# Kernel optimization log

Measured on AMD Instinct MI355X. Metric: run time of the kernel, lower is better.

## Reference

```python
import jax, jax.numpy as jnp
import numpy as np

N_NODES = 100000
N_EDGES = 1600000
IN_CH = 128
OUT_CH = 64


def setup_inputs() -> dict:
    key = jax.random.key(0)
    k1, k2, k3 = jax.random.split(key, 3)
    x = jax.random.normal(k1, (N_NODES, IN_CH), dtype=jnp.float32)
    edge_index = jax.random.randint(k2, (2, N_EDGES), 0, N_NODES, dtype=jnp.int32)
    # Glorot-style init for the GCN weight
    W = jax.random.normal(k3, (IN_CH, OUT_CH), dtype=jnp.float32) * (1.0 / np.sqrt(IN_CH))
    b = jnp.zeros((OUT_CH,), dtype=jnp.float32)
    return {"x": x, "edge_index": edge_index, "W": W, "b": b}


def reference(x, edge_index, W, b):
    # GCNConv (PyG semantics): linear transform, add self loops,
    # symmetric deg^{-1/2} normalization, scatter-add aggregation, bias; then ReLU.
    n = x.shape[0]
    h = x @ W  # [N, out]

    loops = jnp.arange(n, dtype=edge_index.dtype)
    row = jnp.concatenate([edge_index[0], loops])  # source nodes
    col = jnp.concatenate([edge_index[1], loops])  # target nodes

    deg = jax.ops.segment_sum(jnp.ones_like(col, dtype=h.dtype), col, num_segments=n)
    deg_inv_sqrt = jnp.where(deg > 0, jax.lax.rsqrt(jnp.maximum(deg, 1e-12)), 0.0)
    norm = deg_inv_sqrt[row] * deg_inv_sqrt[col]  # [E+N]

    msg = h[row] * norm[:, None]  # gather + scale
    out = jax.ops.segment_sum(msg, col, num_segments=n)  # scatter-add
    return jax.nn.relu(out + b)
```

## Files before the change

kernel.cpp:

```cpp
#include <hip/hip_runtime.h>
#include <hip/hip_fp16.h>

#define INC 128
#define OUTC 64
#define MAXBUK 512
#define CAP 6144

typedef __attribute__((ext_vector_type(8))) short short8;
typedef __attribute__((ext_vector_type(4))) float f32x4;

__device__ __forceinline__ ushort f2bf(float f) {
    union { float f; unsigned u; } v; v.f = f;
    unsigned r = v.u + 0x7FFF + ((v.u >> 16) & 1);
    return (ushort)(r >> 16);
}

__global__ __launch_bounds__(512) void buk_fill_kernel(const int* __restrict__ rowi,
                                                       const int* __restrict__ coli,
                                                       int* __restrict__ cursor,
                                                       int* __restrict__ packed,
                                                       int E, int nbuk, int per) {
    __shared__ int lcnt[MAXBUK];
    __shared__ int lbase[MAXBUK];
    int tid = threadIdx.x;
    int c0 = blockIdx.x * per;
    int c1 = min(E, c0 + per);
    for (int t = tid; t < nbuk; t += 512) lcnt[t] = 0;
    __syncthreads();
    for (int e = c0 + tid; e < c1; e += 512)
        atomicAdd(&lcnt[coli[e] >> 8], 1);
    __syncthreads();
    for (int t = tid; t < nbuk; t += 512) {
        int c = lcnt[t];
        if (c) lbase[t] = atomicAdd(&cursor[t], c);
        lcnt[t] = 0;
    }
    __syncthreads();
    for (int e = c0 + tid; e < c1; e += 512) {
        int s = rowi[e], d = coli[e];
        int bk = d >> 8;
        int pos = lbase[bk] + atomicAdd(&lcnt[bk], 1);
        if (pos < CAP)
            packed[(size_t)bk * CAP + pos] = (s << 8) | (d & 255);
    }
}

__global__ __launch_bounds__(1024) void deg_kernel(const int* __restrict__ packed,
                                                   const int* __restrict__ cursor,
                                                   float* __restrict__ dinv, int n) {
    __shared__ int cnt[256];
    int k = blockIdx.x, tid = threadIdx.x;
    if (tid < 256) cnt[tid] = 0;
    __syncthreads();
    int m = min(cursor[k], CAP);
    const int* pk = packed + (size_t)k * CAP;
    for (int e = tid; e < m; e += 1024)
        atomicAdd(&cnt[pk[e] & 255], 1);
    __syncthreads();
    int node = (k << 8) + tid;
    if (tid < 256 && node < n) dinv[node] = rsqrtf(1.0f + (float)cnt[tid]);
}

#define WT_STRIDE 136
__global__ __launch_bounds__(256) void gemm_kernel(
        const float* __restrict__ x, const float* __restrict__ W,
        const float* __restrict__ dinv, __half2* __restrict__ g2, int n) {
    __shared__ ushort WT[OUTC * WT_STRIDE];
    int tid = threadIdx.x;
    #pragma unroll
    for (int i = 0; i < 8; ++i) {
        int idx4 = tid + i * 256;
        float4 v = ((const float4*)W)[idx4];
        int e = idx4 * 4;
        int k = e >> 6, nn = e & 63;
        WT[(nn + 0) * WT_STRIDE + k] = f2bf(v.x);
        WT[(nn + 1) * WT_STRIDE + k] = f2bf(v.y);
        WT[(nn + 2) * WT_STRIDE + k] = f2bf(v.z);
        WT[(nn + 3) * WT_STRIDE + k] = f2bf(v.w);
    }
    __syncthreads();

    int w = tid >> 6, lane = tid & 63;
    int m = lane & 15, quad = lane >> 4;
    int rbase = blockIdx.x * 128 + w * 32;

    short8 afrag[2][4];
    #pragma unroll
    for (int rt = 0; rt < 2; ++rt) {
        int row = rbase + rt * 16 + m;
        #pragma unroll
        for (int kc = 0; kc < 4; ++kc) {
            float4 v0 = make_float4(0.f, 0.f, 0.f, 0.f), v1 = v0;
            if (row < n) {
                const float* p = x + (size_t)row * INC + kc * 32 + quad * 8;
                v0 = *(const float4*)p;
                v1 = *(const float4*)(p + 4);
            }
            short8 a;
            a[0] = (short)f2bf(v0.x); a[1] = (short)f2bf(v0.y);
            a[2] = (short)f2bf(v0.z); a[3] = (short)f2bf(v0.w);
            a[4] = (short)f2bf(v1.x); a[5] = (short)f2bf(v1.y);
            a[6] = (short)f2bf(v1.z); a[7] = (short)f2bf(v1.w);
            afrag[rt][kc] = a;
        }
    }

    f32x4 acc[2][4];
    #pragma unroll
    for (int rt = 0; rt < 2; ++rt)
        #pragma unroll
        for (int nt = 0; nt < 4; ++nt)
            acc[rt][nt] = (f32x4){0.f, 0.f, 0.f, 0.f};

    #pragma unroll
    for (int nt = 0; nt < 4; ++nt) {
        #pragma unroll
        for (int kc = 0; kc < 4; ++kc) {
            short8 bf = *(const short8*)&WT[(nt * 16 + m) * WT_STRIDE + kc * 32 + quad * 8];
            acc[0][nt] = __builtin_amdgcn_mfma_f32_16x16x32_bf16(afrag[0][kc], bf, acc[0][nt], 0, 0, 0);
            acc[1][nt] = __builtin_amdgcn_mfma_f32_16x16x32_bf16(afrag[1][kc], bf, acc[1][nt], 0, 0, 0);
        }
    }

    #pragma unroll
    for (int rt = 0; rt < 2; ++rt) {
        #pragma unroll
        for (int reg = 0; reg < 4; ++reg) {
            int r2 = rbase + rt * 16 + quad * 4 + reg;
            if (r2 < n) {
                float di = dinv[r2];
                #pragma unroll
                for (int nt = 0; nt < 2; ++nt)
                    g2[(size_t)r2 * 32 + nt * 16 + m] =
                        __floats2half2_rn(acc[rt][nt][reg] * di, acc[rt][nt + 2][reg] * di);
            }
        }
    }
}

__global__ __launch_bounds__(1024) void agg_kernel(const int* __restrict__ packed,
                                                   const int* __restrict__ cursor,
                                                   const __half2* __restrict__ g2,
                                                   const float* __restrict__ b,
                                                   float* __restrict__ out, int n) {
    __shared__ int cnt[256];
    __shared__ int sc[256];
    __shared__ int cur[256];
    __shared__ int lcsr[CAP];
    int k = blockIdx.x, tid = threadIdx.x;
    int r0 = k << 8;
    if (tid < 256) cnt[tid] = 0;
    __syncthreads();
    int m = min(cursor[k], CAP);
    const int* pk = packed + (size_t)k * CAP;
    int pe[(CAP + 1023) / 1024];
    int ne = 0;
    for (int e = tid; e < m; e += 1024) {
        int p = pk[e];
        pe[ne++] = p;
        atomicAdd(&cnt[p & 255], 1);
    }
    __syncthreads();
    int c = (tid < 256) ? cnt[tid] : 0;
    if (tid < 256) sc[tid] = c;
    __syncthreads();
    #pragma unroll
    for (int off = 1; off < 256; off <<= 1) {
        int t = (tid >= off && tid < 256) ? sc[tid - off] : 0;
        __syncthreads();
        if (tid < 256) sc[tid] += t;
        __syncthreads();
    }
    if (tid < 256) cur[tid] = sc[tid] - c;
    __syncthreads();
    for (int i = 0; i < ne; ++i) {
        int p = pe[i];
        int pos = atomicAdd(&cur[p & 255], 1);
        lcsr[pos] = (int)(((unsigned)p) >> 8);
    }
    __syncthreads();

    int w = tid >> 6, lane = tid & 63;
    int l = lane & 31, half = lane >> 5;
    const __half2* gl = g2 + l;
    float bx = b[l], by = b[l + 32];
    for (int cl = w; cl < 256; cl += 16) {
        int e1 = sc[cl];
        int nd = cnt[cl];
        int j = e1 - nd;
        float ax = 0.f, ay = 0.f;
        for (; j + 16 <= e1; j += 16) {
            int s0 = lcsr[j + half];
            int s1 = lcsr[j + 2 + half];
            int s2 = lcsr[j + 4 + half];
            int s3 = lcsr[j + 6 + half];
            int s4 = lcsr[j + 8 + half];
            int s5 = lcsr[j + 10 + half];
            int s6 = lcsr[j + 12 + half];
            int s7 = lcsr[j + 14 + half];
            float2 f0 = __half22float2(gl[(size_t)s0 * 32]);
            float2 f1 = __half22float2(gl[(size_t)s1 * 32]);
            float2 f2 = __half22float2(gl[(size_t)s2 * 32]);
            float2 f3 = __half22float2(gl[(size_t)s3 * 32]);
            float2 f4 = __half22float2(gl[(size_t)s4 * 32]);
            float2 f5 = __half22float2(gl[(size_t)s5 * 32]);
            float2 f6 = __half22float2(gl[(size_t)s6 * 32]);
            float2 f7 = __half22float2(gl[(size_t)s7 * 32]);
            ax += ((f0.x + f1.x) + (f2.x + f3.x)) + ((f4.x + f5.x) + (f6.x + f7.x));
            ay += ((f0.y + f1.y) + (f2.y + f3.y)) + ((f4.y + f5.y) + (f6.y + f7.y));
        }
        if (j + 8 <= e1) {
            int s0 = lcsr[j + half];
            int s1 = lcsr[j + 2 + half];
            int s2 = lcsr[j + 4 + half];
            int s3 = lcsr[j + 6 + half];
            float2 f0 = __half22float2(gl[(size_t)s0 * 32]);
            float2 f1 = __half22float2(gl[(size_t)s1 * 32]);
            float2 f2 = __half22float2(gl[(size_t)s2 * 32]);
            float2 f3 = __half22float2(gl[(size_t)s3 * 32]);
            ax += (f0.x + f1.x) + (f2.x + f3.x);
            ay += (f0.y + f1.y) + (f2.y + f3.y);
            j += 8;
        }
        for (; j + 2 <= e1; j += 2) {
            int s = lcsr[j + half];
            float2 f = __half22float2(gl[(size_t)s * 32]);
            ax += f.x; ay += f.y;
        }
        if (j < e1 && half == 0) {
            int s = lcsr[j];
            float2 f = __half22float2(gl[(size_t)s * 32]);
            ax += f.x; ay += f.y;
        }
        ax += __shfl_xor(ax, 32);
        ay += __shfl_xor(ay, 32);
        int node = r0 + cl;
        if (half == 0 && node < n) {
            float2 s = __half22float2(gl[(size_t)node * 32]);
            float di = rsqrtf(1.0f + (float)nd);
            out[(size_t)node * OUTC + l]      = fmaxf((ax + s.x) * di + bx, 0.f);
            out[(size_t)node * OUTC + 32 + l] = fmaxf((ay + s.y) * di + by, 0.f);
        }
    }
}

extern "C" void kernel_launch(void* const* d_in, const int* in_sizes, int n_in,
                              void* d_out, int out_size, void* d_ws, size_t ws_size,
                              hipStream_t stream) {
    const float* x  = (const float*)d_in[0];
    const int*   ei = (const int*)d_in[1];
    const float* W  = (const float*)d_in[2];
    const float* b  = (const float*)d_in[3];
    float* out = (float*)d_out;

    int n = in_sizes[0] / INC;
    int E = in_sizes[1] / 2;
    const int* rowi = ei;
    const int* coli = ei + E;

    int nbuk = (n + 255) >> 8;
    int n_pad = ((n + 255) / 256) * 256;

    char* ws = (char*)d_ws;
    int*     cursor = (int*)ws;                  ws += (size_t)MAXBUK * 4;
    float*   dinv   = (float*)ws;                ws += (size_t)n_pad * 4;
    int*     packed = (int*)ws;                  ws += (size_t)nbuk * CAP * 4;
    __half2* g2     = (__half2*)ws;

    int fblocks = 512;
    int per = (E + fblocks - 1) / fblocks;

    hipMemsetAsync(cursor, 0, (size_t)MAXBUK * 4, stream);
    buk_fill_kernel<<<fblocks, 512, 0, stream>>>(rowi, coli, cursor, packed, E, nbuk, per);
    deg_kernel<<<nbuk, 1024, 0, stream>>>(packed, cursor, dinv, n);
    gemm_kernel<<<(n + 127) / 128, 256, 0, stream>>>(x, W, dinv, g2, n);
    agg_kernel<<<nbuk, 1024, 0, stream>>>(packed, cursor, g2, b, out, n);
}
```

Before: 172.9 us.

## Fuse degree counting into bucket fill and shrink buckets to 128 nodes

Removes the separate degree kernel: global degree counts are now accumulated with global atomics during bucket fill, and the GEMM and aggregation kernels read them directly. Buckets shrink from 256 to 128 nodes, which gives smaller shared-memory CSR tiles, 512-thread aggregation blocks and more blocks for occupancy. The aggregation prefix scan now runs on the precomputed degrees, and gather offsets are pre-scaled to byte offsets in 32-bit arithmetic. This adds 1.6M global atomics into a 100K-entry array, and the lower per-bucket capacity of 3328 edges raises the risk of overflow on skewed inputs.

```diff
diff --git a/kernel.cpp b/kernel.cpp
--- a/kernel.cpp
+++ b/kernel.cpp
@@ -3,8 +3,9 @@
 
 #define INC 128
 #define OUTC 64
-#define MAXBUK 512
-#define CAP 6144
+#define MAXBUK 1024
+#define BNODES 128
+#define CAP 3328
 
 typedef __attribute__((ext_vector_type(8))) short short8;
 typedef __attribute__((ext_vector_type(4))) float f32x4;
@@ -18,6 +19,7 @@
 __global__ __launch_bounds__(512) void buk_fill_kernel(const int* __restrict__ rowi,
                                                        const int* __restrict__ coli,
                                                        int* __restrict__ cursor,
+                                                       int* __restrict__ degG,
                                                        int* __restrict__ packed,
                                                        int E, int nbuk, int per) {
     __shared__ int lcnt[MAXBUK];
@@ -27,8 +29,11 @@
     int c1 = min(E, c0 + per);
     for (int t = tid; t < nbuk; t += 512) lcnt[t] = 0;
     __syncthreads();
-    for (int e = c0 + tid; e < c1; e += 512)
-        atomicAdd(&lcnt[coli[e] >> 8], 1);
+    for (int e = c0 + tid; e < c1; e += 512) {
+        int d = coli[e];
+        atomicAdd(&lcnt[d >> 7], 1);
+        atomicAdd(&degG[d], 1);
+    }
     __syncthreads();
     for (int t = tid; t < nbuk; t += 512) {
         int c = lcnt[t];
@@ -38,33 +43,17 @@
     __syncthreads();
     for (int e = c0 + tid; e < c1; e += 512) {
         int s = rowi[e], d = coli[e];
-        int bk = d >> 8;
+        int bk = d >> 7;
         int pos = lbase[bk] + atomicAdd(&lcnt[bk], 1);
         if (pos < CAP)
-            packed[(size_t)bk * CAP + pos] = (s << 8) | (d & 255);
-    }
-}
-
-__global__ __launch_bounds__(1024) void deg_kernel(const int* __restrict__ packed,
-                                                   const int* __restrict__ cursor,
-                                                   float* __restrict__ dinv, int n) {
-    __shared__ int cnt[256];
-    int k = blockIdx.x, tid = threadIdx.x;
-    if (tid < 256) cnt[tid] = 0;
-    __syncthreads();
-    int m = min(cursor[k], CAP);
-    const int* pk = packed + (size_t)k * CAP;
-    for (int e = tid; e < m; e += 1024)
-        atomicAdd(&cnt[pk[e] & 255], 1);
-    __syncthreads();
-    int node = (k << 8) + tid;
-    if (tid < 256 && node < n) dinv[node] = rsqrtf(1.0f + (float)cnt[tid]);
+            packed[(size_t)bk * CAP + pos] = (s << 8) | (d & 127);
+    }
 }
 
 #define WT_STRIDE 136
 __global__ __launch_bounds__(256) void gemm_kernel(
         const float* __restrict__ x, const float* __restrict__ W,
-        const float* __restrict__ dinv, __half2* __restrict__ g2, int n) {
+        const int* __restrict__ degG, __half2* __restrict__ g2, int n) {
     __shared__ ushort WT[OUTC * WT_STRIDE];
     int tid = threadIdx.x;
     #pragma unroll
@@ -128,7 +117,7 @@
         for (int reg = 0; reg < 4; ++reg) {
             int r2 = rbase + rt * 16 + quad * 4 + reg;
             if (r2 < n) {
-                float di = dinv[r2];
+                float di = rsqrtf(1.0f + (float)degG[r2]);
                 #pragma unroll
                 for (int nt = 0; nt < 2; ++nt)
                     g2[(size_t)r2 * 32 + nt * 16 + m] =
@@ -138,105 +127,103 @@
     }
 }
 
-__global__ __launch_bounds__(1024) void agg_kernel(const int* __restrict__ packed,
-                                                   const int* __restrict__ cursor,
-                                                   const __half2* __restrict__ g2,
-                                                   const float* __restrict__ b,
-                                                   float* __restrict__ out, int n) {
-    __shared__ int cnt[256];
-    __shared__ int sc[256];
-    __shared__ int cur[256];
+__global__ __launch_bounds__(512) void agg_kernel(const int* __restrict__ packed,
+                                                  const int* __restrict__ cursor,
+                                                  const int* __restrict__ degG,
+                                                  const __half2* __restrict__ g2,
+                                                  const float* __restrict__ b,
+                                                  float* __restrict__ out, int n) {
+    __shared__ int cnt[BNODES];
+    __shared__ int sc[BNODES];
+    __shared__ int cur[BNODES];
     __shared__ int lcsr[CAP];
     int k = blockIdx.x, tid = threadIdx.x;
-    int r0 = k << 8;
-    if (tid < 256) cnt[tid] = 0;
-    __syncthreads();
+    int r0 = k << 7;
+    if (tid < BNODES) {
+        int node = r0 + tid;
+        int c = (node < n) ? degG[node] : 0;
+        cnt[tid] = c;
+        sc[tid] = c;
+    }
+    __syncthreads();
+    #pragma unroll
+    for (int off = 1; off < BNODES; off <<= 1) {
+        int t = (tid >= off && tid < BNODES) ? sc[tid - off] : 0;
+        __syncthreads();
+        if (tid < BNODES) sc[tid] += t;
+        __syncthreads();
+    }
+    if (tid < BNODES) cur[tid] = sc[tid] - cnt[tid];
+    __syncthreads();
+
     int m = min(cursor[k], CAP);
     const int* pk = packed + (size_t)k * CAP;
-    int pe[(CAP + 1023) / 1024];
-    int ne = 0;
-    for (int e = tid; e < m; e += 1024) {
+    for (int e = tid; e < m; e += 512) {
         int p = pk[e];
-        pe[ne++] = p;
-        atomicAdd(&cnt[p & 255], 1);
-    }
-    __syncthreads();
-    int c = (tid < 256) ? cnt[tid] : 0;
-    if (tid < 256) sc[tid] = c;
-    __syncthreads();
-    #pragma unroll
-    for (int off = 1; off < 256; off <<= 1) {
-        int t = (tid >= off && tid < 256) ? sc[tid - off] : 0;
-        __syncthreads();
-        if (tid < 256) sc[tid] += t;
-        __syncthreads();
-    }
-    if (tid < 256) cur[tid] = sc[tid] - c;
-    __syncthreads();
-    for (int i = 0; i < ne; ++i) {
-        int p = pe[i];
-        int pos = atomicAdd(&cur[p & 255], 1);
-        lcsr[pos] = (int)(((unsigned)p) >> 8);
+        int pos = atomicAdd(&cur[p & 127], 1);
+        if (pos < CAP)
+            lcsr[pos] = (int)((((unsigned)p) >> 8) << 7);
     }
     __syncthreads();
 
     int w = tid >> 6, lane = tid & 63;
     int l = lane & 31, half = lane >> 5;
-    const __half2* gl = g2 + l;
+    const char* gbase = (const char*)g2;
+    unsigned lo4 = (unsigned)l * 4u;
     float bx = b[l], by = b[l + 32];
-    for (int cl = w; cl < 256; cl += 16) {
+    for (int cl = w; cl < BNODES; cl += 8) {
         int e1 = sc[cl];
         int nd = cnt[cl];
         int j = e1 - nd;
         float ax = 0.f, ay = 0.f;
         for (; j + 16 <= e1; j += 16) {
-            int s0 = lcsr[j + half];
-            int s1 = lcsr[j + 2 + half];
-            int s2 = lcsr[j + 4 + half];
-            int s3 = lcsr[j + 6 + half];
-            int s4 = lcsr[j + 8 + half];
-            int s5 = lcsr[j + 10 + half];
-            int s6 = lcsr[j + 12 + half];
-            int s7 = lcsr[j + 14 + half];
-            float2 f0 = __half22float2(gl[(size_t)s0 * 32]);
-            float2 f1 = __half22float2(gl[(size_t)s1 * 32]);
-            float2 f2 = __half22float2(gl[(size_t)s2 * 32]);
-            float2 f3 = __half22float2(gl[(size_t)s3 * 32]);
-            float2 f4 = __half22float2(gl[(size_t)s4 * 32]);
-            float2 f5 = __half22float2(gl[(size_t)s5 * 32]);
-            float2 f6 = __half22float2(gl[(size_t)s6 * 32]);
-            float2 f7 = __half22float2(gl[(size_t)s7 * 32]);
+            unsigned o0 = (unsigned)lcsr[j + half]      + lo4;
+            unsigned o1 = (unsigned)lcsr[j + 2 + half]  + lo4;
+            unsigned o2 = (unsigned)lcsr[j + 4 + half]  + lo4;
+            unsigned o3 = (unsigned)lcsr[j + 6 + half]  + lo4;
+            unsigned o4 = (unsigned)lcsr[j + 8 + half]  + lo4;
+            unsigned o5 = (unsigned)lcsr[j + 10 + half] + lo4;
+            unsigned o6 = (unsigned)lcsr[j + 12 + half] + lo4;
+            unsigned o7 = (unsigned)lcsr[j + 14 + half] + lo4;
+            float2 f0 = __half22float2(*(const __half2*)(gbase + o0));
+            float2 f1 = __half22float2(*(const __half2*)(gbase + o1));
+            float2 f2 = __half22float2(*(const __half2*)(gbase + o2));
+            float2 f3 = __half22float2(*(const __half2*)(gbase + o3));
+            float2 f4 = __half22float2(*(const __half2*)(gbase + o4));
+            float2 f5 = __half22float2(*(const __half2*)(gbase + o5));
+            float2 f6 = __half22float2(*(const __half2*)(gbase + o6));
+            float2 f7 = __half22float2(*(const __half2*)(gbase + o7));
             ax += ((f0.x + f1.x) + (f2.x + f3.x)) + ((f4.x + f5.x) + (f6.x + f7.x));
             ay += ((f0.y + f1.y) + (f2.y + f3.y)) + ((f4.y + f5.y) + (f6.y + f7.y));
         }
         if (j + 8 <= e1) {
-            int s0 = lcsr[j + half];
-            int s1 = lcsr[j + 2 + half];
-            int s2 = lcsr[j + 4 + half];
-            int s3 = lcsr[j + 6 + half];
-            float2 f0 = __half22float2(gl[(size_t)s0 * 32]);
-            float2 f1 = __half22float2(gl[(size_t)s1 * 32]);
-            float2 f2 = __half22float2(gl[(size_t)s2 * 32]);
-            float2 f3 = __half22float2(gl[(size_t)s3 * 32]);
+            unsigned o0 = (unsigned)lcsr[j + half]     + lo4;
+            unsigned o1 = (unsigned)lcsr[j + 2 + half] + lo4;
+            unsigned o2 = (unsigned)lcsr[j + 4 + half] + lo4;
+            unsigned o3 = (unsigned)lcsr[j + 6 + half] + lo4;
+            float2 f0 = __half22float2(*(const __half2*)(gbase + o0));
+            float2 f1 = __half22float2(*(const __half2*)(gbase + o1));
+            float2 f2 = __half22float2(*(const __half2*)(gbase + o2));
+            float2 f3 = __half22float2(*(const __half2*)(gbase + o3));
             ax += (f0.x + f1.x) + (f2.x + f3.x);
             ay += (f0.y + f1.y) + (f2.y + f3.y);
             j += 8;
         }
         for (; j + 2 <= e1; j += 2) {
-            int s = lcsr[j + half];
-            float2 f = __half22float2(gl[(size_t)s * 32]);
+            unsigned o = (unsigned)lcsr[j + half] + lo4;
+            float2 f = __half22float2(*(const __half2*)(gbase + o));
             ax += f.x; ay += f.y;
         }
         if (j < e1 && half == 0) {
-            int s = lcsr[j];
-            float2 f = __half22float2(gl[(size_t)s * 32]);
+            unsigned o = (unsigned)lcsr[j] + lo4;
+            float2 f = __half22float2(*(const __half2*)(gbase + o));
             ax += f.x; ay += f.y;
         }
         ax += __shfl_xor(ax, 32);
         ay += __shfl_xor(ay, 32);
         int node = r0 + cl;
         if (half == 0 && node < n) {
-            float2 s = __half22float2(gl[(size_t)node * 32]);
+            float2 s = __half22float2(*(const __half2*)(gbase + (((unsigned)node) << 7) + lo4));
             float di = rsqrtf(1.0f + (float)nd);
             out[(size_t)node * OUTC + l]      = fmaxf((ax + s.x) * di + bx, 0.f);
             out[(size_t)node * OUTC + 32 + l] = fmaxf((ay + s.y) * di + by, 0.f);
@@ -258,21 +245,20 @@
     const int* rowi = ei;
     const int* coli = ei + E;
 
-    int nbuk = (n + 255) >> 8;
+    int nbuk = (n + 127) >> 7;
     int n_pad = ((n + 255) / 256) * 256;
 
     char* ws = (char*)d_ws;
     int*     cursor = (int*)ws;                  ws += (size_t)MAXBUK * 4;
-    float*   dinv   = (float*)ws;                ws += (size_t)n_pad * 4;
+    int*     degG   = (int*)ws;                  ws += (size_t)n_pad * 4;
     int*     packed = (int*)ws;                  ws += (size_t)nbuk * CAP * 4;
     __half2* g2     = (__half2*)ws;
 
-    int fblocks = 512;
+    int fblocks = 1024;
     int per = (E + fblocks - 1) / fblocks;
 
-    hipMemsetAsync(cursor, 0, (size_t)MAXBUK * 4, stream);
-    buk_fill_kernel<<<fblocks, 512, 0, stream>>>(rowi, coli, cursor, packed, E, nbuk, per);
-    deg_kernel<<<nbuk, 1024, 0, stream>>>(packed, cursor, dinv, n);
-    gemm_kernel<<<(n + 127) / 128, 256, 0, stream>>>(x, W, dinv, g2, n);
-    agg_kernel<<<nbuk, 1024, 0, stream>>>(packed, cursor, g2, b, out, n);
-}
+    hipMemsetAsync(cursor, 0, (size_t)(MAXBUK + n_pad) * 4, stream);
+    buk_fill_kernel<<<fblocks, 512, 0, stream>>>(rowi, coli, cursor, degG, packed, E, nbuk, per);
+    gemm_kernel<<<(n + 127) / 128, 256, 0, stream>>>(x, W, degG, g2, n);
+    agg_kernel<<<nbuk, 512, 0, stream>>>(packed, cursor, degG, g2, b, out, n);
+}
```

Measured after the change: 231.5 us. +33.9%, slower.

## Build global CSR in degree kernel and aggregate with wave-per-node grid-stride

Applied to the files above, without the earlier changes.

The per-bucket counting sort moves out of the aggregation kernel into the degree kernel, which now writes a global CSR array holding pre-scaled byte offsets, plus per-node row pointers and degrees. The aggregation kernel becomes a small-block, grid-stride, one-wavefront-per-node loop that reads neighbour offsets from global memory instead of LDS. This drops the 1024-thread blocks with large shared memory, which should raise occupancy and balance the load. The cost is an extra global CSR write and read, and the index loads now go to global memory rather than LDS.

```diff
diff --git a/kernel.cpp b/kernel.cpp
--- a/kernel.cpp
+++ b/kernel.cpp
@@ -45,10 +45,15 @@
     }
 }
 
-__global__ __launch_bounds__(1024) void deg_kernel(const int* __restrict__ packed,
+__global__ __launch_bounds__(1024) void csr_kernel(const int* __restrict__ packed,
                                                    const int* __restrict__ cursor,
+                                                   int* __restrict__ csr,
+                                                   int* __restrict__ rowptr,
+                                                   int* __restrict__ degI,
                                                    float* __restrict__ dinv, int n) {
     __shared__ int cnt[256];
+    __shared__ int sc[256];
+    __shared__ int cur[256];
     int k = blockIdx.x, tid = threadIdx.x;
     if (tid < 256) cnt[tid] = 0;
     __syncthreads();
@@ -57,8 +62,33 @@
     for (int e = tid; e < m; e += 1024)
         atomicAdd(&cnt[pk[e] & 255], 1);
     __syncthreads();
-    int node = (k << 8) + tid;
-    if (tid < 256 && node < n) dinv[node] = rsqrtf(1.0f + (float)cnt[tid]);
+    int c = (tid < 256) ? cnt[tid] : 0;
+    if (tid < 256) sc[tid] = c;
+    __syncthreads();
+    #pragma unroll
+    for (int off = 1; off < 256; off <<= 1) {
+        int t = (tid >= off && tid < 256) ? sc[tid - off] : 0;
+        __syncthreads();
+        if (tid < 256) sc[tid] += t;
+        __syncthreads();
+    }
+    if (tid < 256) {
+        int ex = sc[tid] - c;
+        cur[tid] = ex;
+        int node = (k << 8) + tid;
+        if (node < n) {
+            rowptr[node] = k * CAP + ex;
+            degI[node]   = c;
+            dinv[node]   = rsqrtf(1.0f + (float)c);
+        }
+    }
+    __syncthreads();
+    int* ck = csr + (size_t)k * CAP;
+    for (int e = tid; e < m; e += 1024) {
+        int p = pk[e];
+        int pos = atomicAdd(&cur[p & 255], 1);
+        ck[pos] = (int)((((unsigned)p) >> 8) << 7);
+    }
 }
 
 #define WT_STRIDE 136
@@ -138,105 +168,70 @@
     }
 }
 
-__global__ __launch_bounds__(1024) void agg_kernel(const int* __restrict__ packed,
-                                                   const int* __restrict__ cursor,
-                                                   const __half2* __restrict__ g2,
-                                                   const float* __restrict__ b,
-                                                   float* __restrict__ out, int n) {
-    __shared__ int cnt[256];
-    __shared__ int sc[256];
-    __shared__ int cur[256];
-    __shared__ int lcsr[CAP];
-    int k = blockIdx.x, tid = threadIdx.x;
-    int r0 = k << 8;
-    if (tid < 256) cnt[tid] = 0;
-    __syncthreads();
-    int m = min(cursor[k], CAP);
-    const int* pk = packed + (size_t)k * CAP;
-    int pe[(CAP + 1023) / 1024];
-    int ne = 0;
-    for (int e = tid; e < m; e += 1024) {
-        int p = pk[e];
-        pe[ne++] = p;
-        atomicAdd(&cnt[p & 255], 1);
-    }
-    __syncthreads();
-    int c = (tid < 256) ? cnt[tid] : 0;
-    if (tid < 256) sc[tid] = c;
-    __syncthreads();
-    #pragma unroll
-    for (int off = 1; off < 256; off <<= 1) {
-        int t = (tid >= off && tid < 256) ? sc[tid - off] : 0;
-        __syncthreads();
-        if (tid < 256) sc[tid] += t;
-        __syncthreads();
-    }
-    if (tid < 256) cur[tid] = sc[tid] - c;
-    __syncthreads();
-    for (int i = 0; i < ne; ++i) {
-        int p = pe[i];
-        int pos = atomicAdd(&cur[p & 255], 1);
-        lcsr[pos] = (int)(((unsigned)p) >> 8);
-    }
-    __syncthreads();
-
-    int w = tid >> 6, lane = tid & 63;
+__global__ __launch_bounds__(256) void agg_kernel(const int* __restrict__ csr,
+                                                  const int* __restrict__ rowptr,
+                                                  const int* __restrict__ degI,
+                                                  const __half2* __restrict__ g2,
+                                                  const float* __restrict__ b,
+                                                  float* __restrict__ out, int n, int nwav) {
+    int w = blockIdx.x * 4 + (threadIdx.x >> 6);
+    int lane = threadIdx.x & 63;
     int l = lane & 31, half = lane >> 5;
-    const __half2* gl = g2 + l;
+    const char* gbase = (const char*)g2;
+    unsigned lo4 = (unsigned)l * 4u;
     float bx = b[l], by = b[l + 32];
-    for (int cl = w; cl < 256; cl += 16) {
-        int e1 = sc[cl];
-        int nd = cnt[cl];
-        int j = e1 - nd;
+    for (int node = w; node < n; node += nwav) {
+        int j = rowptr[node];
+        int nd = degI[node];
+        int e1 = j + nd;
+        float2 s = __half22float2(*(const __half2*)(gbase + (((unsigned)node) << 7) + lo4));
         float ax = 0.f, ay = 0.f;
         for (; j + 16 <= e1; j += 16) {
-            int s0 = lcsr[j + half];
-            int s1 = lcsr[j + 2 + half];
-            int s2 = lcsr[j + 4 + half];
-            int s3 = lcsr[j + 6 + half];
-            int s4 = lcsr[j + 8 + half];
-            int s5 = lcsr[j + 10 + half];
-            int s6 = lcsr[j + 12 + half];
-            int s7 = lcsr[j + 14 + half];
-            float2 f0 = __half22float2(gl[(size_t)s0 * 32]);
-            float2 f1 = __half22float2(gl[(size_t)s1 * 32]);
-            float2 f2 = __half22float2(gl[(size_t)s2 * 32]);
-            float2 f3 = __half22float2(gl[(size_t)s3 * 32]);
-            float2 f4 = __half22float2(gl[(size_t)s4 * 32]);
-            float2 f5 = __half22float2(gl[(size_t)s5 * 32]);
-            float2 f6 = __half22float2(gl[(size_t)s6 * 32]);
-            float2 f7 = __half22float2(gl[(size_t)s7 * 32]);
+            unsigned o0 = (unsigned)csr[j + half]      + lo4;
+            unsigned o1 = (unsigned)csr[j + 2 + half]  + lo4;
+            unsigned o2 = (unsigned)csr[j + 4 + half]  + lo4;
+            unsigned o3 = (unsigned)csr[j + 6 + half]  + lo4;
+            unsigned o4 = (unsigned)csr[j + 8 + half]  + lo4;
+            unsigned o5 = (unsigned)csr[j + 10 + half] + lo4;
+            unsigned o6 = (unsigned)csr[j + 12 + half] + lo4;
+            unsigned o7 = (unsigned)csr[j + 14 + half] + lo4;
+            float2 f0 = __half22float2(*(const __half2*)(gbase + o0));
+            float2 f1 = __half22float2(*(const __half2*)(gbase + o1));
+            float2 f2 = __half22float2(*(const __half2*)(gbase + o2));
+            float2 f3 = __half22float2(*(const __half2*)(gbase + o3));
+            float2 f4 = __half22float2(*(const __half2*)(gbase + o4));
+            float2 f5 = __half22float2(*(const __half2*)(gbase + o5));
+            float2 f6 = __half22float2(*(const __half2*)(gbase + o6));
+            float2 f7 = __half22float2(*(const __half2*)(gbase + o7));
             ax += ((f0.x + f1.x) + (f2.x + f3.x)) + ((f4.x + f5.x) + (f6.x + f7.x));
             ay += ((f0.y + f1.y) + (f2.y + f3.y)) + ((f4.y + f5.y) + (f6.y + f7.y));
         }
         if (j + 8 <= e1) {
-            int s0 = lcsr[j + half];
-            int s1 = lcsr[j + 2 + half];
-            int s2 = lcsr[j + 4 + half];
-            int s3 = lcsr[j + 6 + half];
-            float2 f0 = __half22float2(gl[(size_t)s0 * 32]);
-            float2 f1 = __half22float2(gl[(size_t)s1 * 32]);
-            float2 f2 = __half22float2(gl[(size_t)s2 * 32]);
-            float2 f3 = __half22float2(gl[(size_t)s3 * 32]);
+            unsigned o0 = (unsigned)csr[j + half]     + lo4;
+            unsigned o1 = (unsigned)csr[j + 2 + half] + lo4;
+            unsigned o2 = (unsigned)csr[j + 4 + half] + lo4;
+            unsigned o3 = (unsigned)csr[j + 6 + half] + lo4;
+            float2 f0 = __half22float2(*(const __half2*)(gbase + o0));
+            float2 f1 = __half22float2(*(const __half2*)(gbase + o1));
+            float2 f2 = __half22float2(*(const __half2*)(gbase + o2));
+            float2 f3 = __half22float2(*(const __half2*)(gbase + o3));
             ax += (f0.x + f1.x) + (f2.x + f3.x);
             ay += (f0.y + f1.y) + (f2.y + f3.y);
             j += 8;
         }
         for (; j + 2 <= e1; j += 2) {
-            int s = lcsr[j + half];
-            float2 f = __half22float2(gl[(size_t)s * 32]);
+            unsigned o = (unsigned)csr[j + half] + lo4;
+            float2 f = __half22float2(*(const __half2*)(gbase + o));
             ax += f.x; ay += f.y;
         }
         if (j < e1 && half == 0) {
-            int s = lcsr[j];
-            float2 f = __half22float2(gl[(size_t)s * 32]);
+            unsigned o = (unsigned)csr[j] + lo4;
+            float2 f = __half22float2(*(const __half2*)(gbase + o));
             ax += f.x; ay += f.y;
         }
         ax += __shfl_xor(ax, 32);
         ay += __shfl_xor(ay, 32);
-        int node = r0 + cl;
-        if (half == 0 && node < n) {
-            float2 s = __half22float2(gl[(size_t)node * 32]);
+        if (half == 0) {
             float di = rsqrtf(1.0f + (float)nd);
             out[(size_t)node * OUTC + l]      = fmaxf((ax + s.x) * di + bx, 0.f);
             out[(size_t)node * OUTC + 32 + l] = fmaxf((ay + s.y) * di + by, 0.f);
@@ -264,7 +259,10 @@
     char* ws = (char*)d_ws;
     int*     cursor = (int*)ws;                  ws += (size_t)MAXBUK * 4;
     float*   dinv   = (float*)ws;                ws += (size_t)n_pad * 4;
+    int*     degI   = (int*)ws;                  ws += (size_t)n_pad * 4;
+    int*     rowptr = (int*)ws;                  ws += (size_t)n_pad * 4;
     int*     packed = (int*)ws;                  ws += (size_t)nbuk * CAP * 4;
+    int*     csr    = (int*)ws;                  ws += (size_t)nbuk * CAP * 4;
     __half2* g2     = (__half2*)ws;
 
     int fblocks = 512;
@@ -272,7 +270,8 @@
 
     hipMemsetAsync(cursor, 0, (size_t)MAXBUK * 4, stream);
     buk_fill_kernel<<<fblocks, 512, 0, stream>>>(rowi, coli, cursor, packed, E, nbuk, per);
-    deg_kernel<<<nbuk, 1024, 0, stream>>>(packed, cursor, dinv, n);
+    csr_kernel<<<nbuk, 1024, 0, stream>>>(packed, cursor, csr, rowptr, degI, dinv, n);
     gemm_kernel<<<(n + 127) / 128, 256, 0, stream>>>(x, W, dinv, g2, n);
-    agg_kernel<<<nbuk, 1024, 0, stream>>>(packed, cursor, g2, b, out, n);
-}
+    int ablocks = 2048;
+    agg_kernel<<<ablocks, 256, 0, stream>>>(csr, rowptr, degI, g2, b, out, n, ablocks * 4);
+}
```

Measured after the change: 183.4 us. +6.0%, slower.

## Stage bucketed edges in shared memory for coalesced global writes in fill kernel

Applied to the files above, without the earlier changes.

The bucket fill kernel now runs a block-wide prefix scan over per-bucket counts and sorts each block's edge chunk into LDS grouped by bucket. It then writes each bucket's contiguous segment to global memory, so the scattered per-edge global stores become mostly contiguous runs. This adds a 9-step scan with barriers, about 20KB of LDS per block, and a fixed FCH chunk size that assumes per-block edge count at most 3200 and at most 512 buckets.

```diff
diff --git a/kernel.cpp b/kernel.cpp
--- a/kernel.cpp
+++ b/kernel.cpp
@@ -5,6 +5,7 @@
 #define OUTC 64
 #define MAXBUK 512
 #define CAP 6144
+#define FCH 3200
 
 typedef __attribute__((ext_vector_type(8))) short short8;
 typedef __attribute__((ext_vector_type(4))) float f32x4;
@@ -20,28 +21,49 @@
                                                        int* __restrict__ cursor,
                                                        int* __restrict__ packed,
                                                        int E, int nbuk, int per) {
-    __shared__ int lcnt[MAXBUK];
-    __shared__ int lbase[MAXBUK];
+    __shared__ int lcnt[512];
+    __shared__ int sc[512];
+    __shared__ int lbase[512];
+    __shared__ int sp[FCH];
+    __shared__ ushort sb[FCH];
     int tid = threadIdx.x;
     int c0 = blockIdx.x * per;
     int c1 = min(E, c0 + per);
-    for (int t = tid; t < nbuk; t += 512) lcnt[t] = 0;
+    lcnt[tid] = 0;
     __syncthreads();
     for (int e = c0 + tid; e < c1; e += 512)
         atomicAdd(&lcnt[coli[e] >> 8], 1);
     __syncthreads();
-    for (int t = tid; t < nbuk; t += 512) {
-        int c = lcnt[t];
-        if (c) lbase[t] = atomicAdd(&cursor[t], c);
-        lcnt[t] = 0;
-    }
+    int v = lcnt[tid];
+    sc[tid] = v;
+    __syncthreads();
+    #pragma unroll
+    for (int off = 1; off < 512; off <<= 1) {
+        int t = (tid >= off) ? sc[tid - off] : 0;
+        __syncthreads();
+        sc[tid] += t;
+        __syncthreads();
+    }
+    int ex = sc[tid] - v;
+    int gb = 0;
+    if (v) gb = atomicAdd(&cursor[tid], v);
+    lbase[tid] = gb - ex;
+    lcnt[tid] = ex;
     __syncthreads();
     for (int e = c0 + tid; e < c1; e += 512) {
         int s = rowi[e], d = coli[e];
         int bk = d >> 8;
-        int pos = lbase[bk] + atomicAdd(&lcnt[bk], 1);
-        if (pos < CAP)
-            packed[(size_t)bk * CAP + pos] = (s << 8) | (d & 255);
+        int pos = atomicAdd(&lcnt[bk], 1);
+        sp[pos] = (s << 8) | (d & 255);
+        sb[pos] = (ushort)bk;
+    }
+    __syncthreads();
+    int m = c1 - c0;
+    for (int t = tid; t < m; t += 512) {
+        int bk = sb[t];
+        int p = lbase[bk] + t;
+        if (p < CAP)
+            packed[(size_t)bk * CAP + p] = sp[t];
     }
 }
 
@@ -270,7 +292,7 @@
     int fblocks = 512;
     int per = (E + fblocks - 1) / fblocks;
 
-    hipMemsetAsync(cursor, 0, (size_t)MAXBUK * 4, stream);
+    (void)hipMemsetAsync(cursor, 0, (size_t)MAXBUK * 4, stream);
     buk_fill_kernel<<<fblocks, 512, 0, stream>>>(rowi, coli, cursor, packed, E, nbuk, per);
     deg_kernel<<<nbuk, 1024, 0, stream>>>(packed, cursor, dinv, n);
     gemm_kernel<<<(n + 127) / 128, 256, 0, stream>>>(x, W, dinv, g2, n);
```

Result: faster. 169.3 us (-2.1%).
